# Performance work log

Measured on AMD Instinct MI355X. Metric: run time of the kernel, lower is better.

The kernel has to match this reference:

```python
import jax, jax.numpy as jnp
import numpy as np
import math

B, S_TGT, S_SRC, D, H, FF = 4, 2048, 2048, 512, 8, 2048
DK = D // H
EPS = 1e-6


def layernorm(x, gamma, mu):
    # torch: gamma*(x-mean)/(std+eps)+mu with unbiased std (ddof=1), eps OUTSIDE sqrt
    mean = jnp.mean(x, axis=-1, keepdims=True)
    std = jnp.std(x, axis=-1, keepdims=True, ddof=1)
    return gamma * (x - mean) / (std + EPS) + mu


def mha(q, k, v, wq, wk, wv, wo, bo, mask):
    # q:[B,Sq,D] k,v:[B,Sk,D]; weights [D,D] (applied as x@W)
    Bq, Sq, _ = q.shape
    Sk = k.shape[1]
    Q = (q @ wq).reshape(Bq, Sq, H, DK).transpose(0, 2, 1, 3)  # [B,H,Sq,dk]
    K = (k @ wk).reshape(Bq, Sk, H, DK).transpose(0, 2, 1, 3)
    V = (v @ wv).reshape(Bq, Sk, H, DK).transpose(0, 2, 1, 3)
    scores = jnp.einsum('bhqd,bhkd->bhqk', Q, K) / math.sqrt(DK)
    scores = jnp.where(mask == 0, -1e9, scores)
    attn = jax.nn.softmax(scores, axis=-1)
    out = jnp.einsum('bhqk,bhkd->bhqd', attn, V)  # [B,H,Sq,dk]
    out = out.transpose(0, 2, 1, 3).reshape(Bq, Sq, D)
    return out @ wo + bo


def setup_inputs() -> dict:
    key = jax.random.key(0)
    ks = jax.random.split(key, 20)
    sc = 0.02
    inp = {
        'x': jax.random.normal(ks[0], (B, S_TGT, D), jnp.float32),
        'encoder_output': jax.random.normal(ks[1], (B, S_SRC, D), jnp.float32),
        'src_mask': jnp.ones((1, 1, 1, S_SRC), jnp.int32),
        'tgt_mask': jnp.tril(jnp.ones((S_TGT, S_TGT), jnp.int32))[None, None],
        # self-attention params
        'sa_wq': jax.random.normal(ks[2], (D, D)) * sc,
        'sa_wk': jax.random.normal(ks[3], (D, D)) * sc,
        'sa_wv': jax.random.normal(ks[4], (D, D)) * sc,
        'sa_wo': jax.random.normal(ks[5], (D, D)) * sc,
        'sa_bo': jnp.zeros((D,), jnp.float32),
        # cross-attention params
        'ca_wq': jax.random.normal(ks[6], (D, D)) * sc,
        'ca_wk': jax.random.normal(ks[7], (D, D)) * sc,
        'ca_wv': jax.random.normal(ks[8], (D, D)) * sc,
        'ca_wo': jax.random.normal(ks[9], (D, D)) * sc,
        'ca_bo': jnp.zeros((D,), jnp.float32),
        # feed-forward params
        'ff_w1': jax.random.normal(ks[10], (D, FF)) * sc,
        'ff_b1': jnp.zeros((FF,), jnp.float32),
        'ff_w2': jax.random.normal(ks[11], (FF, D)) * sc,
        'ff_b2': jnp.zeros((D,), jnp.float32),
        # layernorm params (3 residual connections)
        'ln0_g': jnp.ones((D,), jnp.float32), 'ln0_b': jnp.zeros((D,), jnp.float32),
        'ln1_g': jnp.ones((D,), jnp.float32), 'ln1_b': jnp.zeros((D,), jnp.float32),
        'ln2_g': jnp.ones((D,), jnp.float32), 'ln2_b': jnp.zeros((D,), jnp.float32),
    }
    return inp


def reference(x, encoder_output, src_mask, tgt_mask,
              sa_wq, sa_wk, sa_wv, sa_wo, sa_bo,
              ca_wq, ca_wk, ca_wv, ca_wo, ca_bo,
              ff_w1, ff_b1, ff_w2, ff_b2,
              ln0_g, ln0_b, ln1_g, ln1_b, ln2_g, ln2_b):
    # pre-LN residual blocks; dropout in eval mode (identity)
    h = layernorm(x, ln0_g, ln0_b)
    x = x + mha(h, h, h, sa_wq, sa_wk, sa_wv, sa_wo, sa_bo, tgt_mask)
    h = layernorm(x, ln1_g, ln1_b)
    x = x + mha(h, encoder_output, encoder_output, ca_wq, ca_wk, ca_wv, ca_wo, ca_bo, src_mask)
    h = layernorm(x, ln2_g, ln2_b)
    ff = jax.nn.relu(h @ ff_w1 + ff_b1) @ ff_w2 + ff_b2
    return x + ff
```

## Files before the change

kernel.cpp:

```cpp
#include <hip/hip_runtime.h>
#include <cstdint>

typedef short s8v __attribute__((ext_vector_type(8)));
typedef short s4v __attribute__((ext_vector_type(4)));
typedef float f4v __attribute__((ext_vector_type(4)));
typedef unsigned int u32;

#define DEV static __device__ __forceinline__

DEV unsigned short f2bf(float f) {
  u32 u = __builtin_bit_cast(u32, f);
  u += 0x7FFF + ((u >> 16) & 1);
  return (unsigned short)(u >> 16);
}

DEV void gload16(const void* g, void* l) {
  __builtin_amdgcn_global_load_lds(
      (const __attribute__((address_space(1))) u32*)g,
      (__attribute__((address_space(3))) u32*)l, 16, 0, 0);
}

struct TransArgs {
  const float* in[10];
  unsigned short* out[10];
};

__global__ __launch_bounds__(256) void trans_all_kernel(TransArgs ta) {
  int id = blockIdx.x;
  int wi, t, K, N, tx, ty;
  if (id < 2048) {
    wi = id >> 8; t = id & 255; K = 512; N = 512; tx = t & 15; ty = t >> 4;
  } else if (id < 3072) {
    wi = 8; t = id - 2048; K = 512; N = 2048; tx = t & 63; ty = t >> 6;
  } else {
    wi = 9; t = id - 3072; K = 2048; N = 512; tx = t & 15; ty = t >> 4;
  }
  const float* in = ta.in[wi];
  unsigned short* out = ta.out[wi];
  __shared__ float tile[32][33];
  int lx = threadIdx.x & 31, ly = threadIdx.x >> 5;
  int bn = tx * 32, bk = ty * 32;
#pragma unroll
  for (int i = 0; i < 32; i += 8)
    tile[ly + i][lx] = in[(size_t)(bk + ly + i) * N + bn + lx];
  __syncthreads();
#pragma unroll
  for (int i = 0; i < 32; i += 8)
    out[(size_t)(bn + ly + i) * K + bk + lx] = f2bf(tile[lx][ly + i]);
}

__global__ __launch_bounds__(256) void cast_kernel(
    const float* __restrict__ in, unsigned short* __restrict__ out, int n8) {
  int i = blockIdx.x * 256 + threadIdx.x;
  if (i >= n8) return;
  const float4* p = (const float4*)(in + (size_t)i * 8);
  float4 a = p[0], b = p[1];
  float va[8] = {a.x, a.y, a.z, a.w, b.x, b.y, b.z, b.w};
  s8v o;
#pragma unroll
  for (int j = 0; j < 8; j++) o[j] = (short)f2bf(va[j]);
  *(s8v*)(out + (size_t)i * 8) = o;
}

__global__ __launch_bounds__(256) void ln_kernel(
    const float* __restrict__ x, const float* __restrict__ g,
    const float* __restrict__ bt, unsigned short* __restrict__ out) {
  int row = blockIdx.x * 4 + (threadIdx.x >> 6);
  int lane = threadIdx.x & 63;
  const float* xr = x + (size_t)row * 512 + lane * 8;
  float4 v0 = *(const float4*)xr;
  float4 v1 = *(const float4*)(xr + 4);
  float va[8] = {v0.x, v0.y, v0.z, v0.w, v1.x, v1.y, v1.z, v1.w};
  float s = 0.f, s2 = 0.f;
#pragma unroll
  for (int j = 0; j < 8; j++) { s += va[j]; s2 += va[j] * va[j]; }
#pragma unroll
  for (int off = 1; off < 64; off <<= 1) {
    s += __shfl_xor(s, off);
    s2 += __shfl_xor(s2, off);
  }
  float mean = s * (1.f / 512.f);
  float var = (s2 - 512.f * mean * mean) * (1.f / 511.f);
  var = fmaxf(var, 0.f);
  float inv = 1.f / (sqrtf(var) + 1e-6f);
  const float* gp = g + lane * 8;
  const float* bp = bt + lane * 8;
  float4 g0 = *(const float4*)gp, g1 = *(const float4*)(gp + 4);
  float4 b0 = *(const float4*)bp, b1 = *(const float4*)(bp + 4);
  float ga[8] = {g0.x, g0.y, g0.z, g0.w, g1.x, g1.y, g1.z, g1.w};
  float ba[8] = {b0.x, b0.y, b0.z, b0.w, b1.x, b1.y, b1.z, b1.w};
  s8v o;
#pragma unroll
  for (int j = 0; j < 8; j++)
    o[j] = (short)f2bf(ga[j] * (va[j] - mean) * inv + ba[j]);
  *(s8v*)(out + (size_t)row * 512 + lane * 8) = o;
}

#define EPI_QKV3 0
#define EPI_Q 1
#define EPI_KV2 2
#define EPI_BIAS_RES 3
#define EPI_RELU 4

#define QSCALE 0.18033688f

template <int EPI, int BN>
__global__ __launch_bounds__(256, 3) void gemm_kernel(
    const unsigned short* __restrict__ A, const unsigned short* __restrict__ Bt,
    const float* __restrict__ bias, const float* __restrict__ res,
    void* __restrict__ out0, void* __restrict__ out1, void* __restrict__ out2,
    int M, int N, int K) {
  __shared__ alignas(16) unsigned short sA[2][128 * 32];
  __shared__ alignas(16) unsigned short sB[2][BN * 32];
  constexpr int NC = BN / 32;
  int tid = threadIdx.x;
  int w = tid >> 6, lane = tid & 63;
  int wm = w >> 1, wn = w & 1;
  int quad = lane >> 4, l15 = lane & 15;

  int lin = blockIdx.x + gridDim.x * blockIdx.y;
  int xcd = lin & 7, j = lin >> 3;
  int bmi = xcd * 8 + (j & 7);
  int bni = j >> 3;
  int bm = bmi * 128, bn = bni * BN;

  int r0 = lane >> 2, c0 = (lane & 3) * 8;
  const unsigned short* gA0 = A + (size_t)(bm + w * 16 + r0) * K + c0;
  const unsigned short* gA1 = gA0 + (size_t)64 * K;
  const unsigned short* gB0 = Bt + (size_t)(bn + w * 16 + r0) * K + c0;
  const unsigned short* gB1 = gB0 + (size_t)64 * K;

  auto prefetch = [&](int k0, int buf) {
    gload16(gA0 + k0, &sA[buf][w * 512]);
    gload16(gA1 + k0, &sA[buf][(w + 4) * 512]);
    gload16(gB0 + k0, &sB[buf][w * 512]);
    if (BN == 128) gload16(gB1 + k0, &sB[buf][(w + 4) * 512]);
  };

  f4v acc[4][NC];
#pragma unroll
  for (int r = 0; r < 4; r++)
#pragma unroll
    for (int c = 0; c < NC; c++) acc[r][c] = {0.f, 0.f, 0.f, 0.f};

  prefetch(0, 0);
  int nk = K >> 5;
  for (int it = 0; it < nk; it++) {
    int buf = it & 1;
    __syncthreads();
    if (it + 1 < nk) prefetch((it + 1) << 5, buf ^ 1);
    s8v af[4], bf[NC];
#pragma unroll
    for (int r = 0; r < 4; r++)
      af[r] = *(const s8v*)&sA[buf][(wm * 64 + r * 16 + l15) * 32 + quad * 8];
#pragma unroll
    for (int c = 0; c < NC; c++)
      bf[c] = *(const s8v*)&sB[buf][(wn * (BN / 2) + c * 16 + l15) * 32 + quad * 8];
#pragma unroll
    for (int r = 0; r < 4; r++)
#pragma unroll
      for (int c = 0; c < NC; c++)
        acc[r][c] = __builtin_amdgcn_mfma_f32_16x16x32_bf16(af[r], bf[c], acc[r][c], 0, 0, 0);
  }

  constexpr int BP = 512 / BN;
  int route = 0;
  if (EPI == EPI_QKV3) route = bni / BP;
  if (EPI == EPI_KV2) route = 1 + bni / BP;
#pragma unroll
  for (int r = 0; r < 4; r++) {
#pragma unroll
    for (int c = 0; c < NC; c++) {
#pragma unroll
      for (int i = 0; i < 4; i++) {
        int row = bm + wm * 64 + r * 16 + quad * 4 + i;
        int col = bn + wn * (BN / 2) + c * 16 + l15;
        float v = acc[r][c][i];
        if (EPI == EPI_BIAS_RES) {
          float* o = (float*)out0;
          o[(size_t)row * N + col] = v + bias[col] + res[(size_t)row * N + col];
        } else if (EPI == EPI_RELU) {
          unsigned short* o = (unsigned short*)out0;
          o[(size_t)row * N + col] = f2bf(fmaxf(v + bias[col], 0.f));
        } else {
          int colq = col & 511;
          int b = row >> 11, s = row & 2047, h = colq >> 6, dk = colq & 63;
          if (route == 0) {
            unsigned short* o = (unsigned short*)out0;
            o[(((size_t)(b * 8 + h) * 2048) + s) * 64 + dk] = f2bf(v * QSCALE);
          } else if (route == 1) {
            unsigned short* o = (unsigned short*)out1;
            o[(((size_t)(b * 8 + h) * 2048) + s) * 64 + dk] = f2bf(v);
          } else {
            unsigned short* o = (unsigned short*)out2;
            o[(((size_t)(b * 8 + h) * 64) + dk) * 2048 + s] = f2bf(v);
          }
        }
      }
    }
  }
}

template <int CAUSAL>
__global__ __launch_bounds__(256, 2) void attn_kernel(
    const unsigned short* __restrict__ Q, const unsigned short* __restrict__ Kk,
    const unsigned short* __restrict__ Vt,
    unsigned short* __restrict__ out) {
  const int S = 2048;
  __shared__ alignas(16) unsigned short sK[2][64 * 64];
  __shared__ alignas(16) unsigned short sV[2][64 * 64];
  __shared__ alignas(16) unsigned short sO[128 * 68];
  int bh = blockIdx.x;
  int qt = CAUSAL ? ((int)gridDim.y - 1 - blockIdx.y) : blockIdx.y;
  int b = bh >> 3, h = bh & 7;
  int tid = threadIdx.x;
  int w = tid >> 6, lane = tid & 63;
  int quad = lane >> 4, l15 = lane & 15;

  const unsigned short* Qp = Q + (size_t)bh * S * 64;
  const unsigned short* Kp = Kk + (size_t)bh * S * 64;
  const unsigned short* Vp = Vt + (size_t)bh * 64 * S;

  s8v bq[2][2];
#pragma unroll
  for (int qb = 0; qb < 2; qb++) {
    const unsigned short* qr =
        Qp + (size_t)(qt * 128 + w * 32 + qb * 16 + l15) * 64 + quad * 8;
    bq[qb][0] = *(const s8v*)qr;
    bq[qb][1] = *(const s8v*)(qr + 32);
  }

  int rowA = ((l15 >> 2) * 8) + (l15 & 3);
  int koff[2][2][2];
#pragma unroll
  for (int win = 0; win < 2; win++)
#pragma unroll
    for (int half = 0; half < 2; half++) {
      int row = win * 32 + half * 4 + rowA;
      int h7 = (row & 7) ^ (((row >> 3) & 1) << 2);
      koff[win][half][0] = row * 64 + ((quad ^ h7) << 3);
      koff[win][half][1] = row * 64 + (((4 + quad) ^ h7) << 3);
    }
  int voff[4][2];
#pragma unroll
  for (int c2 = 0; c2 < 4; c2++) {
    int row = c2 * 16 + l15;
    int h7 = (row & 7) ^ (((row >> 3) & 1) << 2);
#pragma unroll
    for (int win = 0; win < 2; win++)
      voff[c2][win] = row * 64 + ((((win * 4) + quad) ^ h7) << 3);
  }
  int st_row[2], st_lds[2], st_cc[2];
#pragma unroll
  for (int c = 0; c < 2; c++) {
    int row = c * 32 + (tid >> 3), cc = tid & 7;
    int slot = cc ^ (row & 7) ^ (((row >> 3) & 1) << 2);
    st_row[c] = row;
    st_cc[c] = cc;
    st_lds[c] = row * 64 + slot * 8;
  }

  float l_lane[2] = {0.f, 0.f};
  f4v oacc[2][4];
#pragma unroll
  for (int qb = 0; qb < 2; qb++)
#pragma unroll
    for (int c2 = 0; c2 < 4; c2++) oacc[qb][c2] = {0.f, 0.f, 0.f, 0.f};

  int ntiles = CAUSAL ? (2 * qt + 2) : (S / 64);

  s8v rk[2][2], rv[2][2];
  auto load_set = [&](int t, int set) {
    int kb = t * 64;
#pragma unroll
    for (int c = 0; c < 2; c++) {
      rk[set][c] = *(const s8v*)(Kp + (size_t)(kb + st_row[c]) * 64 + st_cc[c] * 8);
      rv[set][c] = *(const s8v*)(Vp + (size_t)st_row[c] * S + kb + st_cc[c] * 8);
    }
  };
  auto write_set = [&](int buf, int set) {
#pragma unroll
    for (int c = 0; c < 2; c++) {
      *(s8v*)&sK[buf][st_lds[c]] = rk[set][c];
      *(s8v*)&sV[buf][st_lds[c]] = rv[set][c];
    }
  };

  auto compute = [&](int buf, int t) {
    f4v sacc[2][2][2];
#pragma unroll
    for (int qb = 0; qb < 2; qb++)
#pragma unroll
      for (int win = 0; win < 2; win++)
#pragma unroll
        for (int half = 0; half < 2; half++) sacc[qb][win][half] = {0.f, 0.f, 0.f, 0.f};
#pragma unroll
    for (int win = 0; win < 2; win++)
#pragma unroll
      for (int half = 0; half < 2; half++) {
        s8v a0 = *(const s8v*)&sK[buf][koff[win][half][0]];
        s8v a1 = *(const s8v*)&sK[buf][koff[win][half][1]];
#pragma unroll
        for (int qb = 0; qb < 2; qb++) {
          sacc[qb][win][half] =
              __builtin_amdgcn_mfma_f32_16x16x32_bf16(a0, bq[qb][0], sacc[qb][win][half], 0, 0, 0);
          sacc[qb][win][half] =
              __builtin_amdgcn_mfma_f32_16x16x32_bf16(a1, bq[qb][1], sacc[qb][win][half], 0, 0, 0);
        }
      }

    if (CAUSAL && t >= 2 * qt) {
      int toff = (t - 2 * qt) * 64;
#pragma unroll
      for (int qb = 0; qb < 2; qb++) {
        int qloc = w * 32 + qb * 16 + l15;
#pragma unroll
        for (int win = 0; win < 2; win++)
#pragma unroll
          for (int half = 0; half < 2; half++)
#pragma unroll
            for (int i = 0; i < 4; i++)
              if (toff + win * 32 + quad * 8 + half * 4 + i > qloc)
                sacc[qb][win][half][i] = -1e9f;
      }
    }

    s8v bp[2][2];
#pragma unroll
    for (int qb = 0; qb < 2; qb++)
#pragma unroll
      for (int win = 0; win < 2; win++) {
        float p[8];
#pragma unroll
        for (int half = 0; half < 2; half++)
#pragma unroll
          for (int i = 0; i < 4; i++) {
            float e = __builtin_exp2f(sacc[qb][win][half][i]);
            p[half * 4 + i] = e;
            l_lane[qb] += e;
          }
        int4 pk;
#pragma unroll
        for (int jj = 0; jj < 4; jj++)
          pk[jj] = (int)__builtin_amdgcn_perm(
              __builtin_bit_cast(u32, p[2 * jj + 1]),
              __builtin_bit_cast(u32, p[2 * jj]), 0x07060302u);
        bp[qb][win] = __builtin_bit_cast(s8v, pk);
      }

#pragma unroll
    for (int c2 = 0; c2 < 4; c2++)
#pragma unroll
      for (int win = 0; win < 2; win++) {
        s8v av = *(const s8v*)&sV[buf][voff[c2][win]];
#pragma unroll
        for (int qb = 0; qb < 2; qb++)
          oacc[qb][c2] =
              __builtin_amdgcn_mfma_f32_16x16x32_bf16(av, bp[qb][win], oacc[qb][c2], 0, 0, 0);
      }
  };

  load_set(0, 0);
  write_set(0, 0);
  load_set(1, 1);

  for (int t = 0; t < ntiles; t += 2) {
    __syncthreads();
    if (t + 2 < ntiles) load_set(t + 2, 0);
    compute(0, t);
    write_set(1, 1);
    __syncthreads();
    if (t + 3 < ntiles) load_set(t + 3, 1);
    compute(1, t + 1);
    if (t + 2 < ntiles) write_set(0, 0);
  }

#pragma unroll
  for (int qb = 0; qb < 2; qb++) {
    float l = l_lane[qb];
    l += __shfl_xor(l, 16);
    l += __shfl_xor(l, 32);
    float inv = 1.f / l;
#pragma unroll
    for (int c2 = 0; c2 < 4; c2++) {
      s4v o;
#pragma unroll
      for (int i = 0; i < 4; i++) o[i] = (short)f2bf(oacc[qb][c2][i] * inv);
      *(s4v*)&sO[(w * 32 + qb * 16 + l15) * 68 + c2 * 16 + quad * 4] = o;
    }
  }
  __syncthreads();
#pragma unroll
  for (int c = 0; c < 4; c++) {
    int idx = c * 256 + tid;
    int r = idx >> 3, ch = idx & 7;
    s8v v = *(const s8v*)&sO[r * 68 + ch * 8];
    *(s8v*)(out + ((size_t)(b * S + qt * 128 + r) * 512) + h * 64 + ch * 8) = v;
  }
}

extern "C" void kernel_launch(void* const* d_in, const int* in_sizes, int n_in,
                              void* d_out, int out_size, void* d_ws, size_t ws_size,
                              hipStream_t stream) {
  const float* x = (const float*)d_in[0];
  const float* enc = (const float*)d_in[1];
  const float* sa_wq = (const float*)d_in[4];
  const float* sa_wk = (const float*)d_in[5];
  const float* sa_wv = (const float*)d_in[6];
  const float* sa_wo = (const float*)d_in[7];
  const float* sa_bo = (const float*)d_in[8];
  const float* ca_wq = (const float*)d_in[9];
  const float* ca_wk = (const float*)d_in[10];
  const float* ca_wv = (const float*)d_in[11];
  const float* ca_wo = (const float*)d_in[12];
  const float* ca_bo = (const float*)d_in[13];
  const float* ff_w1 = (const float*)d_in[14];
  const float* ff_b1 = (const float*)d_in[15];
  const float* ff_w2 = (const float*)d_in[16];
  const float* ff_b2 = (const float*)d_in[17];
  const float* ln0_g = (const float*)d_in[18];
  const float* ln0_b = (const float*)d_in[19];
  const float* ln1_g = (const float*)d_in[20];
  const float* ln1_b = (const float*)d_in[21];
  const float* ln2_g = (const float*)d_in[22];
  const float* ln2_b = (const float*)d_in[23];
  float* out = (float*)d_out;

  const int M = 8192;

  size_t off = 0;
  auto carve = [&](size_t bytes) -> void* {
    void* r = (char*)d_ws + off;
    off += (bytes + 255) & ~(size_t)255;
    return r;
  };
  unsigned short* swqT = (unsigned short*)carve(512 * 512 * 2);
  unsigned short* swkT = (unsigned short*)carve(512 * 512 * 2);
  unsigned short* swvT = (unsigned short*)carve(512 * 512 * 2);
  unsigned short* swoT = (unsigned short*)carve(512 * 512 * 2);
  unsigned short* cwqT = (unsigned short*)carve(512 * 512 * 2);
  unsigned short* cwkT = (unsigned short*)carve(512 * 512 * 2);
  unsigned short* cwvT = (unsigned short*)carve(512 * 512 * 2);
  unsigned short* cwoT = (unsigned short*)carve(512 * 512 * 2);
  unsigned short* w1T = (unsigned short*)carve((size_t)2048 * 512 * 2);
  unsigned short* w2T = (unsigned short*)carve((size_t)512 * 2048 * 2);
  unsigned short* enc_bf = (unsigned short*)carve((size_t)M * 512 * 2);
  unsigned short* h_bf = (unsigned short*)carve((size_t)M * 512 * 2);
  unsigned short* Qb = (unsigned short*)carve((size_t)M * 512 * 2);
  unsigned short* Kb = (unsigned short*)carve((size_t)M * 512 * 2);
  unsigned short* Vtb = (unsigned short*)carve((size_t)M * 512 * 2);
  unsigned short* attn_bf = (unsigned short*)carve((size_t)M * 512 * 2);
  float* x1 = (float*)carve((size_t)M * 512 * 4);
  unsigned short* f1 = (unsigned short*)carve((size_t)M * 2048 * 2);

  dim3 blk(256);

  TransArgs ta;
  ta.in[0] = sa_wq; ta.out[0] = swqT;
  ta.in[1] = sa_wk; ta.out[1] = swkT;
  ta.in[2] = sa_wv; ta.out[2] = swvT;
  ta.in[3] = sa_wo; ta.out[3] = swoT;
  ta.in[4] = ca_wq; ta.out[4] = cwqT;
  ta.in[5] = ca_wk; ta.out[5] = cwkT;
  ta.in[6] = ca_wv; ta.out[6] = cwvT;
  ta.in[7] = ca_wo; ta.out[7] = cwoT;
  ta.in[8] = ff_w1; ta.out[8] = w1T;
  ta.in[9] = ff_w2; ta.out[9] = w2T;
  trans_all_kernel<<<dim3(4096), blk, 0, stream>>>(ta);
  cast_kernel<<<dim3(M * 512 / 8 / 256), blk, 0, stream>>>(enc, enc_bf, M * 512 / 8);

  dim3 gProj(8, 64);
  dim3 gQKV(12, 64);
  dim3 gKV(16, 64);
  dim3 gFF1(16, 64);
  dim3 gAttn(32, 16);
  dim3 gLN(M / 4);

  ln_kernel<<<gLN, blk, 0, stream>>>(x, ln0_g, ln0_b, h_bf);
  gemm_kernel<EPI_QKV3, 128><<<gQKV, blk, 0, stream>>>(h_bf, swqT, nullptr, nullptr, Qb, Kb, Vtb, M, 1536, 512);
  attn_kernel<1><<<gAttn, blk, 0, stream>>>(Qb, Kb, Vtb, attn_bf);
  gemm_kernel<EPI_BIAS_RES, 64><<<gProj, blk, 0, stream>>>(attn_bf, swoT, sa_bo, x, x1, nullptr, nullptr, M, 512, 512);

  ln_kernel<<<gLN, blk, 0, stream>>>(x1, ln1_g, ln1_b, h_bf);
  gemm_kernel<EPI_Q, 64><<<gProj, blk, 0, stream>>>(h_bf, cwqT, nullptr, nullptr, Qb, nullptr, nullptr, M, 512, 512);
  gemm_kernel<EPI_KV2, 64><<<gKV, blk, 0, stream>>>(enc_bf, cwkT, nullptr, nullptr, nullptr, Kb, Vtb, M, 1024, 512);
  attn_kernel<0><<<gAttn, blk, 0, stream>>>(Qb, Kb, Vtb, attn_bf);
  gemm_kernel<EPI_BIAS_RES, 64><<<gProj, blk, 0, stream>>>(attn_bf, cwoT, ca_bo, x1, x1, nullptr, nullptr, M, 512, 512);

  ln_kernel<<<gLN, blk, 0, stream>>>(x1, ln2_g, ln2_b, h_bf);
  gemm_kernel<EPI_RELU, 128><<<gFF1, blk, 0, stream>>>(h_bf, w1T, ff_b1, nullptr, f1, nullptr, nullptr, M, 2048, 512);
  gemm_kernel<EPI_BIAS_RES, 64><<<gProj, blk, 0, stream>>>(f1, w2T, ff_b2, x1, out, nullptr, nullptr, M, 512, 2048);
}
```

Baseline: 392.7 us.

## Shrink attention LDS and registers to allow four blocks per CU

Places the K/V double buffers and the output staging tile in one shared array, with the output staging reusing the K/V space after the loop. Shared memory per block drops from about 49KB to 32KB. The two-stage register prefetch (two register sets, loop unrolled by two) becomes a single prefetch set with a per-tile loop. Launch bounds go from 2 to 4 blocks per SM, trading prefetch depth and register headroom for occupancy, which risks spills or less latency hiding.

```diff
diff --git a/kernel.cpp b/kernel.cpp
--- a/kernel.cpp
+++ b/kernel.cpp
@@ -202,14 +202,12 @@
 }
 
 template <int CAUSAL>
-__global__ __launch_bounds__(256, 2) void attn_kernel(
+__global__ __launch_bounds__(256, 4) void attn_kernel(
     const unsigned short* __restrict__ Q, const unsigned short* __restrict__ Kk,
     const unsigned short* __restrict__ Vt,
     unsigned short* __restrict__ out) {
   const int S = 2048;
-  __shared__ alignas(16) unsigned short sK[2][64 * 64];
-  __shared__ alignas(16) unsigned short sV[2][64 * 64];
-  __shared__ alignas(16) unsigned short sO[128 * 68];
+  __shared__ alignas(16) unsigned short SB[16384];
   int bh = blockIdx.x;
   int qt = CAUSAL ? ((int)gridDim.y - 1 - blockIdx.y) : blockIdx.y;
   int b = bh >> 3, h = bh & 7;
@@ -269,24 +267,32 @@
 
   int ntiles = CAUSAL ? (2 * qt + 2) : (S / 64);
 
-  s8v rk[2][2], rv[2][2];
-  auto load_set = [&](int t, int set) {
-    int kb = t * 64;
-#pragma unroll
-    for (int c = 0; c < 2; c++) {
-      rk[set][c] = *(const s8v*)(Kp + (size_t)(kb + st_row[c]) * 64 + st_cc[c] * 8);
-      rv[set][c] = *(const s8v*)(Vp + (size_t)st_row[c] * S + kb + st_cc[c] * 8);
-    }
-  };
-  auto write_set = [&](int buf, int set) {
-#pragma unroll
-    for (int c = 0; c < 2; c++) {
-      *(s8v*)&sK[buf][st_lds[c]] = rk[set][c];
-      *(s8v*)&sV[buf][st_lds[c]] = rv[set][c];
-    }
-  };
-
-  auto compute = [&](int buf, int t) {
+  s8v rk[2], rv[2];
+#pragma unroll
+  for (int c = 0; c < 2; c++) {
+    rk[c] = *(const s8v*)(Kp + (size_t)st_row[c] * 64 + st_cc[c] * 8);
+    rv[c] = *(const s8v*)(Vp + (size_t)st_row[c] * S + st_cc[c] * 8);
+  }
+#pragma unroll
+  for (int c = 0; c < 2; c++) {
+    *(s8v*)&SB[st_lds[c]] = rk[c];
+    *(s8v*)&SB[4096 + st_lds[c]] = rv[c];
+  }
+
+  for (int t = 0; t < ntiles; t++) {
+    int buf = t & 1;
+    const unsigned short* sK = &SB[buf * 8192];
+    const unsigned short* sV = sK + 4096;
+    __syncthreads();
+    if (t + 1 < ntiles) {
+      int kb = (t + 1) * 64;
+#pragma unroll
+      for (int c = 0; c < 2; c++) {
+        rk[c] = *(const s8v*)(Kp + (size_t)(kb + st_row[c]) * 64 + st_cc[c] * 8);
+        rv[c] = *(const s8v*)(Vp + (size_t)st_row[c] * S + kb + st_cc[c] * 8);
+      }
+    }
+
     f4v sacc[2][2][2];
 #pragma unroll
     for (int qb = 0; qb < 2; qb++)
@@ -298,8 +304,8 @@
     for (int win = 0; win < 2; win++)
 #pragma unroll
       for (int half = 0; half < 2; half++) {
-        s8v a0 = *(const s8v*)&sK[buf][koff[win][half][0]];
-        s8v a1 = *(const s8v*)&sK[buf][koff[win][half][1]];
+        s8v a0 = *(const s8v*)&sK[koff[win][half][0]];
+        s8v a1 = *(const s8v*)&sK[koff[win][half][1]];
 #pragma unroll
         for (int qb = 0; qb < 2; qb++) {
           sacc[qb][win][half] =
@@ -352,29 +358,25 @@
     for (int c2 = 0; c2 < 4; c2++)
 #pragma unroll
       for (int win = 0; win < 2; win++) {
-        s8v av = *(const s8v*)&sV[buf][voff[c2][win]];
+        s8v av = *(const s8v*)&sV[voff[c2][win]];
 #pragma unroll
         for (int qb = 0; qb < 2; qb++)
           oacc[qb][c2] =
               __builtin_amdgcn_mfma_f32_16x16x32_bf16(av, bp[qb][win], oacc[qb][c2], 0, 0, 0);
       }
-  };
-
-  load_set(0, 0);
-  write_set(0, 0);
-  load_set(1, 1);
-
-  for (int t = 0; t < ntiles; t += 2) {
-    __syncthreads();
-    if (t + 2 < ntiles) load_set(t + 2, 0);
-    compute(0, t);
-    write_set(1, 1);
-    __syncthreads();
-    if (t + 3 < ntiles) load_set(t + 3, 1);
-    compute(1, t + 1);
-    if (t + 2 < ntiles) write_set(0, 0);
-  }
-
+
+    if (t + 1 < ntiles) {
+      unsigned short* dK = &SB[(buf ^ 1) * 8192];
+#pragma unroll
+      for (int c = 0; c < 2; c++) {
+        *(s8v*)&dK[st_lds[c]] = rk[c];
+        *(s8v*)&dK[4096 + st_lds[c]] = rv[c];
+      }
+    }
+  }
+
+  __syncthreads();
+  unsigned short* sO = SB;
 #pragma unroll
   for (int qb = 0; qb < 2; qb++) {
     float l = l_lane[qb];
```

After: 452.0 us. 15.1% more time.
